# Performance work log

Hardware: AMD Instinct MI355X
Metric: run time of the kernel (lower is better)

Reference implementation:

```python
import jax, jax.numpy as jnp
import numpy as np

E, N, D = 800000, 50000, 64

def setup_inputs() -> dict:
    key = jax.random.key(0)
    k0, k1, k2, k3 = jax.random.split(key, 4)
    return {
        "edge_attrs": jax.random.normal(k0, (E, D), dtype=jnp.float32),
        "proj_W": jax.random.normal(k1, (D, D), dtype=jnp.float32) / np.float32(np.sqrt(D)),
        "proj_b": jnp.zeros((D,), dtype=jnp.float32),
        "upd_W": jax.random.normal(k2, (D, D), dtype=jnp.float32) / np.float32(np.sqrt(D)),
        "upd_b": jnp.zeros((D,), dtype=jnp.float32),
        "dst": jax.random.randint(k3, (E,), 0, N, dtype=jnp.int32),
        "n_nodes": N,
    }

def reference(edge_attrs, proj_W, proj_b, upd_W, upd_b, dst, n_nodes):
    # Project each edge attribute: node_projectors[e.type](e.data)
    proj = edge_attrs @ proj_W + proj_b                      # [E, D]
    # Mean-aggregate incoming edges per destination node (MeanAggregator)
    summed = jax.ops.segment_sum(proj, dst, num_segments=n_nodes)          # [N, D]
    counts = jax.ops.segment_sum(jnp.ones((dst.shape[0], 1), proj.dtype),
                                 dst, num_segments=n_nodes)                # [N, 1]
    aggregated = summed / jnp.maximum(counts, 1.0)           # nodes w/o edges -> 0
    # Per-node update: updaters(aggregated)
    return aggregated @ upd_W + upd_b                        # [N, D]
```

## Files before the change

kernel.cpp:

```cpp
#include <hip/hip_runtime.h>
#include <hip/hip_bf16.h>

#define D 64

__global__ void zero_kernel(int4* __restrict__ p, int n4) {
    int i = blockIdx.x * blockDim.x + threadIdx.x;
    if (i < n4) p[i] = make_int4(0, 0, 0, 0);
}

__global__ void count_kernel(const int4* __restrict__ dst4, int* __restrict__ counts, int E4) {
    int i = blockIdx.x * blockDim.x + threadIdx.x;
    if (i < E4) {
        int4 d = dst4[i];
        atomicAdd(&counts[d.x], 1);
        atomicAdd(&counts[d.y], 1);
        atomicAdd(&counts[d.z], 1);
        atomicAdd(&counts[d.w], 1);
    }
}

__global__ void blocksum_kernel(const int* __restrict__ counts, int* __restrict__ bsums, int N) {
    int t = threadIdx.x;
    int i = blockIdx.x * 256 + t;
    int v = (i < N) ? counts[i] : 0;
    int lane = t & 63, wave = t >> 6;
    #pragma unroll
    for (int o = 1; o < 64; o <<= 1) v += __shfl_xor(v, o);
    __shared__ int ws[4];
    if (lane == 0) ws[wave] = v;
    __syncthreads();
    if (t == 0) bsums[blockIdx.x] = ws[0] + ws[1] + ws[2] + ws[3];
}

__global__ void blockscan_kernel(const int* __restrict__ bsums, int* __restrict__ boffs,
                                 int* __restrict__ offsets, int N, int nb,
                                 const float* __restrict__ Wp, const float* __restrict__ Wu,
                                 const float* __restrict__ bp,
                                 float* __restrict__ Wc, float* __restrict__ bc) {
    __shared__ int wsum[16];
    int t = threadIdx.x;
    int wave = t >> 6, lane = t & 63;
    int v = (t < nb) ? bsums[t] : 0;
    int s = v;
    #pragma unroll
    for (int off = 1; off < 64; off <<= 1) {
        int x = __shfl_up(s, off);
        if (lane >= off) s += x;
    }
    if (lane == 63) wsum[wave] = s;
    __syncthreads();
    int wbase = 0, total = 0;
    #pragma unroll
    for (int w = 0; w < 16; ++w) {
        int x = wsum[w];
        total += x;
        if (w < wave) wbase += x;
    }
    if (t < nb) boffs[t] = s - v + wbase;
    if (t == 0) offsets[N] = total;

    for (int idx = t; idx < D * D; idx += 1024) {
        int d = idx >> 6, j = idx & 63;
        float acc = 0.f;
        #pragma unroll
        for (int k = 0; k < D; ++k) acc = fmaf(Wp[d * D + k], Wu[k * D + j], acc);
        Wc[idx] = acc;
    }
    if (t < D) {
        float acc = 0.f;
        #pragma unroll
        for (int k = 0; k < D; ++k) acc = fmaf(bp[k], Wu[k * D + t], acc);
        bc[t] = acc;
    }
}

__global__ void scatter_scan_kernel(const int* __restrict__ counts, const int* __restrict__ boffs,
                                    int* __restrict__ offsets, int* __restrict__ cursor, int N) {
    int t = threadIdx.x;
    int i = blockIdx.x * 256 + t;
    int v = (i < N) ? counts[i] : 0;
    int lane = t & 63, wave = t >> 6;
    int s = v;
    #pragma unroll
    for (int off = 1; off < 64; off <<= 1) {
        int x = __shfl_up(s, off);
        if (lane >= off) s += x;
    }
    __shared__ int ws[4];
    if (lane == 63) ws[wave] = s;
    __syncthreads();
    int wbase = 0;
    #pragma unroll
    for (int w = 0; w < 4; ++w) if (w < wave) wbase += ws[w];
    int excl = s - v + wbase + boffs[blockIdx.x];
    if (i < N) { offsets[i] = excl; cursor[i] = excl; }
}

__global__ void fill_kernel(const int4* __restrict__ dst4, int* __restrict__ cursor,
                            int* __restrict__ csr, int E4) {
    int i = blockIdx.x * blockDim.x + threadIdx.x;
    if (i < E4) {
        int4 d = dst4[i];
        int e = i * 4;
        csr[atomicAdd(&cursor[d.x], 1)] = e + 0;
        csr[atomicAdd(&cursor[d.y], 1)] = e + 1;
        csr[atomicAdd(&cursor[d.z], 1)] = e + 2;
        csr[atomicAdd(&cursor[d.w], 1)] = e + 3;
    }
}

__global__ __launch_bounds__(256) void node_kernel(
        const float4* __restrict__ attrs4, const int* __restrict__ csr,
        const int* __restrict__ offsets,
        const float* __restrict__ Wc, const float* __restrict__ bc,
        const float* __restrict__ ub, float* __restrict__ out, int N) {
    __shared__ float wlds[D * D];
    __shared__ float blds[D];
    __shared__ float ulds[D];
    __shared__ int soff[5];
    int t = threadIdx.x;
    int nbase = blockIdx.x * 4;
    if (t < 5) {
        int nn = nbase + t;
        soff[t] = offsets[(nn <= N) ? nn : N];
    }
    #pragma unroll
    for (int i = t; i < D * D; i += 256) wlds[i] = Wc[i];
    if (t < D) { blds[t] = bc[t]; ulds[t] = ub[t]; }
    __syncthreads();

    int wave = t >> 6, lane = t & 63;
    int n = nbase + wave;
    if (n >= N) return;

    int off = soff[wave];
    int cnt = soff[wave + 1] - off;

    int g = lane >> 4;
    int q = lane & 15;

    float4 acc0 = make_float4(0.f, 0.f, 0.f, 0.f);
    float4 acc1 = make_float4(0.f, 0.f, 0.f, 0.f);
    for (int base = 0; base < cnt; base += 64) {
        int m = cnt - base; if (m > 64) m = 64;
        int idxv = (lane < m) ? csr[off + base + lane] : 0;
        int jj = 0;
        for (; jj + 8 <= m; jj += 8) {
            int e0 = __shfl(idxv, jj + g);
            int e1 = __shfl(idxv, jj + 4 + g);
            float4 a0 = attrs4[(size_t)e0 * 16 + q];
            float4 a1 = attrs4[(size_t)e1 * 16 + q];
            acc0.x += a0.x; acc0.y += a0.y; acc0.z += a0.z; acc0.w += a0.w;
            acc1.x += a1.x; acc1.y += a1.y; acc1.z += a1.z; acc1.w += a1.w;
        }
        for (; jj < m; jj += 4) {
            int sel = jj + g;
            int e = __shfl(idxv, sel);
            if (sel < m) {
                float4 a = attrs4[(size_t)e * 16 + q];
                acc0.x += a.x; acc0.y += a.y; acc0.z += a.z; acc0.w += a.w;
            }
        }
    }
    float4 acc = make_float4(acc0.x + acc1.x, acc0.y + acc1.y,
                             acc0.z + acc1.z, acc0.w + acc1.w);
    acc.x += __shfl_xor(acc.x, 16); acc.y += __shfl_xor(acc.y, 16);
    acc.z += __shfl_xor(acc.z, 16); acc.w += __shfl_xor(acc.w, 16);
    acc.x += __shfl_xor(acc.x, 32); acc.y += __shfl_xor(acc.y, 32);
    acc.z += __shfl_xor(acc.z, 32); acc.w += __shfl_xor(acc.w, 32);

    float inv = (cnt > 0) ? 1.f / (float)cnt : 0.f;
    float marr[4] = { acc.x * inv, acc.y * inv, acc.z * inv, acc.w * inv };

    float accO = ulds[lane] + ((cnt > 0) ? blds[lane] : 0.f);
    #pragma unroll
    for (int d = 0; d < D; ++d) {
        float mv = __shfl(marr[d & 3], d >> 2);
        accO = fmaf(mv, wlds[d * D + lane], accO);
    }
    out[(size_t)n * D + lane] = accO;
}

extern "C" void kernel_launch(void* const* d_in, const int* in_sizes, int n_in,
                              void* d_out, int out_size, void* d_ws, size_t ws_size,
                              hipStream_t stream) {
    const float* edge_attrs = (const float*)d_in[0];
    const float* proj_W     = (const float*)d_in[1];
    const float* proj_b     = (const float*)d_in[2];
    const float* upd_W      = (const float*)d_in[3];
    const float* upd_b      = (const float*)d_in[4];
    const int*   dst        = (const int*)d_in[5];

    const int E = in_sizes[0] / D;
    const int N = out_size / D;
    const int nb = (N + 255) / 256;
    const int E4 = E / 4;
    const int N4 = N / 4;

    int*   counts  = (int*)d_ws;
    int*   offsets = counts + N;
    int*   cursor  = offsets + N + 1;
    int*   bsums   = cursor + N;
    int*   boffs   = bsums + nb;
    int*   csr     = boffs + nb;
    float* Wc      = (float*)(csr + E);
    float* bc      = Wc + D * D;

    zero_kernel<<<(N4 + 255) / 256, 256, 0, stream>>>((int4*)counts, N4);
    count_kernel<<<(E4 + 255) / 256, 256, 0, stream>>>((const int4*)dst, counts, E4);
    blocksum_kernel<<<nb, 256, 0, stream>>>(counts, bsums, N);
    blockscan_kernel<<<1, 1024, 0, stream>>>(bsums, boffs, offsets, N, nb,
                                             proj_W, upd_W, proj_b, Wc, bc);
    scatter_scan_kernel<<<nb, 256, 0, stream>>>(counts, boffs, offsets, cursor, N);
    fill_kernel<<<(E4 + 255) / 256, 256, 0, stream>>>((const int4*)dst, cursor, csr, E4);

    int blocks_n = (N + 3) / 4;
    node_kernel<<<blocks_n, 256, 0, stream>>>((const float4*)edge_attrs, csr, offsets,
                                              Wc, bc, upd_b, (float*)d_out, N);
}
```

Before: 170.8 us.

## Merge three-pass prefix scan into one single-block int4 scan kernel

Replaces the blocksum, blockscan and scatter-scan kernels with one 1024-thread single-block kernel that scans the counts in int4 chunks with a running carry, writing offsets and cursors directly. The weight-combine matmul now stages Wp and Wu in shared memory instead of reading them from global memory. This removes two kernel launches and their inter-kernel gaps. The cost is that about 13 chunks of serial scan now run on a single CU.

```diff
diff --git a/kernel.cpp b/kernel.cpp
--- a/kernel.cpp
+++ b/kernel.cpp
@@ -2,6 +2,8 @@
 #include <hip/hip_bf16.h>
 
 #define D 64
+
+typedef float f32x4 __attribute__((ext_vector_type(4)));
 
 __global__ void zero_kernel(int4* __restrict__ p, int n4) {
     int i = blockIdx.x * blockDim.x + threadIdx.x;
@@ -19,81 +21,70 @@
     }
 }
 
-__global__ void blocksum_kernel(const int* __restrict__ counts, int* __restrict__ bsums, int N) {
+__global__ void scan4_kernel(const int4* __restrict__ counts4, int N4, int N,
+                             int4* __restrict__ offsets4, int4* __restrict__ cursor4,
+                             int* __restrict__ offsets,
+                             const float* __restrict__ Wp, const float* __restrict__ Wu,
+                             const float* __restrict__ bp,
+                             float* __restrict__ Wc, float* __restrict__ bc) {
+    __shared__ int wsum[16];
+    __shared__ float wu[D * D];
+    __shared__ float wp[D * D];
     int t = threadIdx.x;
-    int i = blockIdx.x * 256 + t;
-    int v = (i < N) ? counts[i] : 0;
-    int lane = t & 63, wave = t >> 6;
-    #pragma unroll
-    for (int o = 1; o < 64; o <<= 1) v += __shfl_xor(v, o);
-    __shared__ int ws[4];
-    if (lane == 0) ws[wave] = v;
+    for (int i = t; i < D * D; i += 1024) { wu[i] = Wu[i]; wp[i] = Wp[i]; }
+
+    int wave = t >> 6, lane = t & 63;
+    int carry = 0;
+    int nchunk = (N4 + 1023) / 1024;
+    for (int ch = 0; ch < nchunk; ++ch) {
+        int i = ch * 1024 + t;
+        int4 v = make_int4(0, 0, 0, 0);
+        if (i < N4) v = counts4[i];
+        int vs = v.x + v.y + v.z + v.w;
+        int s = vs;
+        #pragma unroll
+        for (int off = 1; off < 64; off <<= 1) {
+            int x = __shfl_up(s, off);
+            if (lane >= off) s += x;
+        }
+        if (lane == 63) wsum[wave] = s;
+        __syncthreads();
+        int wbase = 0, total = 0;
+        #pragma unroll
+        for (int w = 0; w < 16; ++w) {
+            int x = wsum[w];
+            total += x;
+            if (w < wave) wbase += x;
+        }
+        if (i < N4) {
+            int e0 = s - vs + wbase + carry;
+            int4 o;
+            o.x = e0;
+            o.y = e0 + v.x;
+            o.z = o.y + v.y;
+            o.w = o.z + v.z;
+            offsets4[i] = o;
+            cursor4[i] = o;
+        }
+        carry += total;
+        __syncthreads();
+    }
+    if (t == 0) offsets[N] = carry;
+
     __syncthreads();
-    if (t == 0) bsums[blockIdx.x] = ws[0] + ws[1] + ws[2] + ws[3];
-}
-
-__global__ void blockscan_kernel(const int* __restrict__ bsums, int* __restrict__ boffs,
-                                 int* __restrict__ offsets, int N, int nb,
-                                 const float* __restrict__ Wp, const float* __restrict__ Wu,
-                                 const float* __restrict__ bp,
-                                 float* __restrict__ Wc, float* __restrict__ bc) {
-    __shared__ int wsum[16];
-    int t = threadIdx.x;
-    int wave = t >> 6, lane = t & 63;
-    int v = (t < nb) ? bsums[t] : 0;
-    int s = v;
-    #pragma unroll
-    for (int off = 1; off < 64; off <<= 1) {
-        int x = __shfl_up(s, off);
-        if (lane >= off) s += x;
-    }
-    if (lane == 63) wsum[wave] = s;
-    __syncthreads();
-    int wbase = 0, total = 0;
-    #pragma unroll
-    for (int w = 0; w < 16; ++w) {
-        int x = wsum[w];
-        total += x;
-        if (w < wave) wbase += x;
-    }
-    if (t < nb) boffs[t] = s - v + wbase;
-    if (t == 0) offsets[N] = total;
-
     for (int idx = t; idx < D * D; idx += 1024) {
         int d = idx >> 6, j = idx & 63;
         float acc = 0.f;
         #pragma unroll
-        for (int k = 0; k < D; ++k) acc = fmaf(Wp[d * D + k], Wu[k * D + j], acc);
+        for (int k = 0; k < D; ++k) acc = fmaf(wp[d * D + k], wu[k * D + j], acc);
         Wc[idx] = acc;
     }
     if (t < D) {
         float acc = 0.f;
         #pragma unroll
-        for (int k = 0; k < D; ++k) acc = fmaf(bp[k], Wu[k * D + t], acc);
+        for (int k = 0; k < D; ++k) acc = fmaf(bp[k], wu[k * D + t], acc);
         bc[t] = acc;
     }
-}
-
-__global__ void scatter_scan_kernel(const int* __restrict__ counts, const int* __restrict__ boffs,
-                                    int* __restrict__ offsets, int* __restrict__ cursor, int N) {
-    int t = threadIdx.x;
-    int i = blockIdx.x * 256 + t;
-    int v = (i < N) ? counts[i] : 0;
-    int lane = t & 63, wave = t >> 6;
-    int s = v;
-    #pragma unroll
-    for (int off = 1; off < 64; off <<= 1) {
-        int x = __shfl_up(s, off);
-        if (lane >= off) s += x;
-    }
-    __shared__ int ws[4];
-    if (lane == 63) ws[wave] = s;
-    __syncthreads();
-    int wbase = 0;
-    #pragma unroll
-    for (int w = 0; w < 4; ++w) if (w < wave) wbase += ws[w];
-    int excl = s - v + wbase + boffs[blockIdx.x];
-    if (i < N) { offsets[i] = excl; cursor[i] = excl; }
 }
 
 __global__ void fill_kernel(const int4* __restrict__ dst4, int* __restrict__ cursor,
@@ -193,25 +184,22 @@
 
     const int E = in_sizes[0] / D;
     const int N = out_size / D;
-    const int nb = (N + 255) / 256;
     const int E4 = E / 4;
-    const int N4 = N / 4;
+    const int N4 = (N + 3) / 4;
+    const int Npad = N4 * 4 + 4;
 
     int*   counts  = (int*)d_ws;
-    int*   offsets = counts + N;
-    int*   cursor  = offsets + N + 1;
-    int*   bsums   = cursor + N;
-    int*   boffs   = bsums + nb;
-    int*   csr     = boffs + nb;
+    int*   offsets = counts + Npad;
+    int*   cursor  = offsets + Npad;
+    int*   csr     = cursor + Npad;
     float* Wc      = (float*)(csr + E);
     float* bc      = Wc + D * D;
 
     zero_kernel<<<(N4 + 255) / 256, 256, 0, stream>>>((int4*)counts, N4);
     count_kernel<<<(E4 + 255) / 256, 256, 0, stream>>>((const int4*)dst, counts, E4);
-    blocksum_kernel<<<nb, 256, 0, stream>>>(counts, bsums, N);
-    blockscan_kernel<<<1, 1024, 0, stream>>>(bsums, boffs, offsets, N, nb,
-                                             proj_W, upd_W, proj_b, Wc, bc);
-    scatter_scan_kernel<<<nb, 256, 0, stream>>>(counts, boffs, offsets, cursor, N);
+    scan4_kernel<<<1, 1024, 0, stream>>>((const int4*)counts, N4, N,
+                                         (int4*)offsets, (int4*)cursor, offsets,
+                                         proj_W, upd_W, proj_b, Wc, bc);
     fill_kernel<<<(E4 + 255) / 256, 256, 0, stream>>>((const int4*)dst, cursor, csr, E4);
 
     int blocks_n = (N + 3) / 4;
```

New measurement: 174.0 us. No clear change (+1.8%).
